# Performance work log

Measured on AMD Instinct MI355X. Metric: run time of the kernel, lower is better.

## Reference

```python
import jax, jax.numpy as jnp
import numpy as np

DIM = 256
HEADS = 8
HD = DIM // HEADS
SR = 2
SCALE = HD ** -0.5
EPS = 1e-5


def _layernorm(t, g, b):
    m = jnp.mean(t, axis=-1, keepdims=True)
    v = jnp.mean((t - m) ** 2, axis=-1, keepdims=True)
    return (t - m) / jnp.sqrt(v + EPS) * g + b


def _sr_kv(t, H, W, sr_w, sr_b, ln_g, ln_b, Wkv):
    # t: [B, N, C] with N == H*W -> spatial-reduction conv -> LN -> kv proj
    B, N, C = t.shape
    img = t.transpose(0, 2, 1).reshape(B, C, H, W)
    red = jax.lax.conv_general_dilated(
        img, sr_w, window_strides=(SR, SR), padding='VALID',
        dimension_numbers=('NCHW', 'OIHW', 'NCHW')) + sr_b[None, :, None, None]
    red = red.reshape(B, C, -1).transpose(0, 2, 1)  # [B, Nr, C]
    red = _layernorm(red, ln_g, ln_b)
    Nr = red.shape[1]
    kv = (red @ Wkv).reshape(B, Nr, 2, HEADS, HD).transpose(2, 0, 3, 1, 4)
    return kv[0], kv[1]  # k, v: [B, h, Nr, d]


def _q_heads(t, Wq):
    B, N, _ = t.shape
    return (t @ Wq).reshape(B, N, HEADS, HD).transpose(0, 2, 1, 3)  # [B,h,N,d]


def _attn_out(q, k, v, proj_w, proj_b):
    a = jnp.einsum('bhqd,bhkd->bhqk', q, k) * SCALE
    a = jax.nn.softmax(a, axis=-1)
    o = jnp.einsum('bhqk,bhkd->bhqd', a, v)
    B, h, N, d = o.shape
    return o.transpose(0, 2, 1, 3).reshape(B, N, h * d) @ proj_w + proj_b


def _forward(x, y, Wq, Wkv, sr_w, sr_b, ln_g, ln_b, proj_w, proj_b,
             H_x, W_x, H_y, W_y):
    # B_x == 1 branch of the original module (static shapes)
    B_y = y.shape[0]
    q_x = _q_heads(x, Wq)
    q_y = _q_heads(y, Wq)
    k_x, v_x = _sr_kv(x, H_x, W_x, sr_w, sr_b, ln_g, ln_b, Wkv)
    k_y, v_y = _sr_kv(y, H_y, W_y, sr_w, sr_b, ln_g, ln_b, Wkv)
    # x attends to its own KV + batch-averaged support KV
    k_cat_x = jnp.concatenate([k_x, jnp.mean(k_y, axis=0, keepdims=True)], axis=2)
    v_cat_x = jnp.concatenate([v_x, jnp.mean(v_y, axis=0, keepdims=True)], axis=2)
    x_out = _attn_out(q_x, k_cat_x, v_cat_x, proj_w, proj_b)
    # each support attends to repeated query KV + its own KV
    k_cat_y = jnp.concatenate([jnp.broadcast_to(k_x, (B_y,) + k_x.shape[1:]), k_y], axis=2)
    v_cat_y = jnp.concatenate([jnp.broadcast_to(v_x, (B_y,) + v_x.shape[1:]), v_y], axis=2)
    y_out = _attn_out(q_y, k_cat_y, v_cat_y, proj_w, proj_b)
    return x_out, y_out


def setup_inputs() -> dict:
    key = jax.random.key(0)
    ks = jax.random.split(key, 6)
    std = 0.02
    return {
        'x': jax.random.normal(ks[0], (1, 6400, DIM), jnp.float32),
        'y': jax.random.normal(ks[1], (4, 1024, DIM), jnp.float32),
        'Wq': jax.random.normal(ks[2], (DIM, DIM), jnp.float32) * std,
        'Wkv': jax.random.normal(ks[3], (DIM, 2 * DIM), jnp.float32) * std,
        'sr_w': jax.random.normal(ks[4], (DIM, DIM, SR, SR), jnp.float32) * np.sqrt(2.0 / (SR * SR * DIM)),
        'sr_b': jnp.zeros((DIM,), jnp.float32),
        'ln_g': jnp.ones((DIM,), jnp.float32),
        'ln_b': jnp.zeros((DIM,), jnp.float32),
        'proj_w': jax.random.normal(ks[5], (DIM, DIM), jnp.float32) * std,
        'proj_b': jnp.zeros((DIM,), jnp.float32),
        'H_x': 80, 'W_x': 80, 'H_y': 32, 'W_y': 32,
    }


def reference(x, y, Wq, Wkv, sr_w, sr_b, ln_g, ln_b, proj_w, proj_b,
              H_x, W_x, H_y, W_y):
    return _forward(x, y, Wq, Wkv, sr_w, sr_b, ln_g, ln_b, proj_w, proj_b,
                    H_x, W_x, H_y, W_y)
```

## Files before the change

### kernel.cpp

```cpp
#include <hip/hip_runtime.h>
#include <math.h>

#define DIM 256
#define HD 32
#define KSCALE (0.17677669529663687f * 1.44269504088896340736f)
#define EPS 1e-5f

typedef __attribute__((ext_vector_type(8))) short short8;
typedef __attribute__((ext_vector_type(4))) float f32x4;

union U8 { uint4 u; short8 s; };

__device__ inline unsigned short f2bf(float f) {
    union { float f; unsigned u; } v; v.f = f;
    unsigned r = v.u + 0x7FFF + ((v.u >> 16) & 1);
    return (unsigned short)(r >> 16);
}
__device__ inline float bf2f(unsigned short h) {
    union { unsigned u; float f; } v; v.u = ((unsigned)h) << 16;
    return v.f;
}
__device__ inline unsigned pk2bf(float a, float b) {
    unsigned ua = __float_as_uint(a) + 0x8000u;
    unsigned ub = __float_as_uint(b) + 0x8000u;
    return __builtin_amdgcn_perm(ub, ua, 0x07060302u);
}
__device__ inline uint4 pk8bf(float4 a, float4 b) {
    return make_uint4(pk2bf(a.x, a.y), pk2bf(a.z, a.w),
                      pk2bf(b.x, b.y), pk2bf(b.z, b.w));
}
__device__ inline void up2(unsigned u, float& a, float& b) {
    a = __uint_as_float(u << 16);
    b = __uint_as_float(u & 0xffff0000u);
}
__device__ inline void gl_lds16(const unsigned short* g, unsigned short* l) {
    __builtin_amdgcn_global_load_lds(
        (const __attribute__((address_space(1))) unsigned int*)g,
        (__attribute__((address_space(3))) unsigned int*)l, 16, 0, 0);
}
#define MFMA16(a, b, c) __builtin_amdgcn_mfma_f32_16x16x32_bf16(a, b, c, 0, 0, 0)
#define EXP2(x) __builtin_amdgcn_exp2f(x)

__global__ __launch_bounds__(256) void prep_w(
    const float* __restrict__ Wq, const float* __restrict__ Wkv,
    const float* __restrict__ projw, const float* __restrict__ srw,
    unsigned short* __restrict__ WqT, unsigned short* __restrict__ WkvT,
    unsigned short* __restrict__ projT, unsigned short* __restrict__ BwT)
{
    int idx = blockIdx.x * 256 + threadIdx.x;
    if (idx < 65536) { int n = idx >> 8, k = idx & 255; WqT[idx] = f2bf(Wq[(k << 8) + n]); return; }
    idx -= 65536;
    if (idx < 131072) { int n = idx >> 8, k = idx & 255; WkvT[idx] = f2bf(Wkv[(k << 9) + n]); return; }
    idx -= 131072;
    if (idx < 65536) { int n = idx >> 8, k = idx & 255; projT[idx] = f2bf(projw[(k << 8) + n]); return; }
    idx -= 65536;
    { int o = idx >> 10, rem = idx & 1023, q = rem >> 8, i = rem & 255;
      BwT[idx] = f2bf(srw[(o << 10) + (i << 2) + q]); }
}

__global__ __launch_bounds__(256) void convq_kernel(
    const float* __restrict__ x, const float* __restrict__ y,
    const unsigned short* __restrict__ BwT, const float* __restrict__ srb,
    const unsigned short* __restrict__ WqT,
    unsigned short* __restrict__ redx, unsigned short* __restrict__ redy,
    unsigned short* __restrict__ qxb, unsigned short* __restrict__ qyb)
{
    __shared__ __align__(16) unsigned short At[64][32];
    __shared__ __align__(16) unsigned short Btile[64][32];
    const int tid = threadIdx.x;
    const int lane = tid & 63, w = tid >> 6;
    const int c = lane & 15, quad = lane >> 4;
    const int srow = tid >> 2, sch = (tid & 3) << 3;
    const int bid = blockIdx.x;
    f32x4 acc[4] = {};
    const int rl = (w << 4) + (quad << 2);

    if (bid < 164) {
        const int n0 = (bid & 3) << 6, myi = bid >> 2;
        const float* Xb; unsigned short* Cb; int W, W2, m0;
        if (myi < 25) { Xb = x; Cb = redx; W = 80; W2 = 40; m0 = myi * 64; }
        else {
            const int r = myi - 25, b = r >> 2;
            Xb = y + (size_t)b * 262144; Cb = redy + (size_t)b * 65536;
            W = 32; W2 = 16; m0 = (r & 3) * 64;
        }
        const int p = m0 + srow;
        const int oy = p / W2, ox = p - oy * W2;
        const unsigned short* Bp = BwT + (size_t)(n0 + srow) * 1024 + sch;

        auto addrA = [&](int k0) {
            const int qq = k0 >> 8;
            const int rrow = (2 * oy + (qq >> 1)) * W + 2 * ox + (qq & 1);
            return Xb + (size_t)rrow * DIM + (k0 & 255) + sch;
        };

        const float* ap = addrA(0);
        float4 a0 = *(const float4*)ap, a1 = *(const float4*)(ap + 4);
        uint4 bn = *(const uint4*)Bp;
        for (int k0 = 0; k0 < 1024; k0 += 32) {
            *(uint4*)&At[srow][sch]    = pk8bf(a0, a1);
            *(uint4*)&Btile[srow][sch] = bn;
            if (k0 < 992) {
                const float* np = addrA(k0 + 32);
                a0 = *(const float4*)np; a1 = *(const float4*)(np + 4);
                bn = *(const uint4*)(Bp + k0 + 32);
            }
            __syncthreads();
            short8 a = *(short8*)&At[(w << 4) + c][quad << 3];
            #pragma unroll
            for (int nb = 0; nb < 4; ++nb) {
                short8 b = *(short8*)&Btile[(nb << 4) + c][quad << 3];
                acc[nb] = MFMA16(a, b, acc[nb]);
            }
            __syncthreads();
        }
        #pragma unroll
        for (int nb = 0; nb < 4; ++nb) {
            const int col = n0 + (nb << 4) + c;
            const float bv = srb[col];
            #pragma unroll
            for (int r = 0; r < 4; ++r)
                Cb[(size_t)(m0 + rl + r) * DIM + col] = f2bf(acc[nb][r] + bv);
        }
    } else {
        const int r = bid - 164;
        const int n0 = (r & 3) << 6, mg = (r >> 2) << 6;
        const float* Ab = (mg < 6400) ? x + (size_t)mg * 256
                                      : y + (size_t)(mg - 6400) * 256;
        unsigned short* Cb = (mg < 6400) ? qxb + (size_t)mg * 256
                                         : qyb + (size_t)(mg - 6400) * 256;
        const float* Ap = Ab + (size_t)srow * 256 + sch;
        const unsigned short* Bp = WqT + (size_t)(n0 + srow) * 256 + sch;

        float4 a0 = *(const float4*)Ap, a1 = *(const float4*)(Ap + 4);
        uint4 bn = *(const uint4*)Bp;
        for (int k0 = 0; k0 < 256; k0 += 32) {
            *(uint4*)&At[srow][sch]    = pk8bf(a0, a1);
            *(uint4*)&Btile[srow][sch] = bn;
            if (k0 < 224) {
                a0 = *(const float4*)(Ap + k0 + 32);
                a1 = *(const float4*)(Ap + k0 + 36);
                bn = *(const uint4*)(Bp + k0 + 32);
            }
            __syncthreads();
            short8 a = *(short8*)&At[(w << 4) + c][quad << 3];
            #pragma unroll
            for (int nb = 0; nb < 4; ++nb) {
                short8 b = *(short8*)&Btile[(nb << 4) + c][quad << 3];
                acc[nb] = MFMA16(a, b, acc[nb]);
            }
            __syncthreads();
        }
        #pragma unroll
        for (int nb = 0; nb < 4; ++nb) {
            const int col = n0 + (nb << 4) + c;
            #pragma unroll
            for (int r = 0; r < 4; ++r)
                Cb[(size_t)(rl + r) * 256 + col] = f2bf(acc[nb][r]);
        }
    }
}

__global__ __launch_bounds__(256) void kvln_kernel(
    const unsigned short* __restrict__ redx, const unsigned short* __restrict__ redy,
    const unsigned short* __restrict__ WkvT,
    const float* __restrict__ g, const float* __restrict__ bta,
    unsigned short* __restrict__ kswx, unsigned short* __restrict__ vswx,
    unsigned short* __restrict__ kswy, unsigned short* __restrict__ vswy)
{
    __shared__ __align__(16) unsigned short At[64][32];
    __shared__ __align__(16) unsigned short Btile[64][32];
    const int tid = threadIdx.x;
    const int lane = tid & 63, w = tid >> 6;
    const int c = lane & 15, quad = lane >> 4;
    const int srow = tid >> 2, sch = (tid & 3) << 3;
    const int bid = blockIdx.x;
    const int n0 = (bid & 7) << 6, mg = (bid >> 3) << 6;
    const unsigned short* Ab = (mg < 1600) ? redx + (size_t)mg * 256
                                           : redy + (size_t)(mg - 1600) * 256;
    const unsigned short* Arow = Ab + (size_t)srow * 256 + sch;

    uint4 araw[8];
    float s1 = 0.f, s2 = 0.f;
    #pragma unroll
    for (int ci = 0; ci < 8; ++ci) {
        araw[ci] = *(const uint4*)(Arow + (ci << 5));
        const unsigned* du = (const unsigned*)&araw[ci];
        #pragma unroll
        for (int dd = 0; dd < 4; ++dd) {
            float a, b; up2(du[dd], a, b);
            s1 += a + b; s2 += a * a + b * b;
        }
    }
    s1 += __shfl_xor(s1, 1); s1 += __shfl_xor(s1, 2);
    s2 += __shfl_xor(s2, 1); s2 += __shfl_xor(s2, 2);
    const float mean = s1 * (1.0f / 256.0f);
    const float var  = s2 * (1.0f / 256.0f) - mean * mean;
    const float rstd = rsqrtf(var + EPS);

    #pragma unroll
    for (int ci = 0; ci < 8; ++ci) {
        const int ch = (ci << 5) + sch;
        float4 g0 = *(const float4*)(g + ch),   g1 = *(const float4*)(g + ch + 4);
        float4 b0 = *(const float4*)(bta + ch), b1 = *(const float4*)(bta + ch + 4);
        const unsigned* du = (const unsigned*)&araw[ci];
        float v[8];
        #pragma unroll
        for (int dd = 0; dd < 4; ++dd) up2(du[dd], v[2 * dd], v[2 * dd + 1]);
        float4 o0 = make_float4(fmaf((v[0] - mean) * rstd, g0.x, b0.x),
                                fmaf((v[1] - mean) * rstd, g0.y, b0.y),
                                fmaf((v[2] - mean) * rstd, g0.z, b0.z),
                                fmaf((v[3] - mean) * rstd, g0.w, b0.w));
        float4 o1 = make_float4(fmaf((v[4] - mean) * rstd, g1.x, b1.x),
                                fmaf((v[5] - mean) * rstd, g1.y, b1.y),
                                fmaf((v[6] - mean) * rstd, g1.z, b1.z),
                                fmaf((v[7] - mean) * rstd, g1.w, b1.w));
        araw[ci] = pk8bf(o0, o1);
    }

    const unsigned short* Bp = WkvT + (size_t)(n0 + srow) * 256 + sch;
    uint4 bn = *(const uint4*)Bp;
    f32x4 acc[4] = {};
    for (int k0 = 0; k0 < 256; k0 += 32) {
        *(uint4*)&At[srow][sch]    = araw[k0 >> 5];
        *(uint4*)&Btile[srow][sch] = bn;
        if (k0 < 224) bn = *(const uint4*)(Bp + k0 + 32);
        __syncthreads();
        short8 a = *(short8*)&At[(w << 4) + c][quad << 3];
        #pragma unroll
        for (int nb = 0; nb < 4; ++nb) {
            short8 b = *(short8*)&Btile[(nb << 4) + c][quad << 3];
            acc[nb] = MFMA16(a, b, acc[nb]);
        }
        __syncthreads();
    }

    const int rl = (w << 4) + (quad << 2);
    const int r0 = mg - 1600;
    const int half = rl >> 5, kl0 = rl & 31;
    const int vkeyoff = (half << 10) + (((kl0 >> 2) & 3) << 7) + ((kl0 >> 4) << 2);
    #pragma unroll
    for (int nb = 0; nb < 4; ++nb) {
        const int col = n0 + (nb << 4) + c;
        if (col < 256) {
            const int hh = col >> 5, d = col & 31;
            unsigned short* base = (mg < 1600)
                ? kswx + ((size_t)(hh * 25 + (mg >> 6)) << 11)
                : kswy + ((size_t)(r0 >> 8) << 16) + ((size_t)((hh << 2) + ((r0 >> 6) & 3)) << 11);
            unsigned short* dst = base + (((d >> 3) << 9)) + (d & 7);
            #pragma unroll
            for (int r = 0; r < 4; ++r)
                dst[(rl + r) << 3] = f2bf(acc[nb][r] * KSCALE);
        } else {
            const int hd = col - 256, hv = hd >> 5, d = hd & 31;
            unsigned short* base = (mg < 1600)
                ? vswx + ((size_t)(hv * 25 + (mg >> 6)) << 11)
                : vswy + ((size_t)(r0 >> 8) << 16) + ((size_t)((hv << 2) + ((r0 >> 6) & 3)) << 11);
            unsigned lo = (unsigned)f2bf(acc[nb][0]) | ((unsigned)f2bf(acc[nb][1]) << 16);
            unsigned hi = (unsigned)f2bf(acc[nb][2]) | ((unsigned)f2bf(acc[nb][3]) << 16);
            *(uint2*)(base + vkeyoff + ((d >> 4) << 9) + ((d & 15) << 3)) =
                make_uint2(lo, hi);
        }
    }
}

__global__ __launch_bounds__(256) void kvmean_kernel(
    const unsigned short* __restrict__ kswy, const unsigned short* __restrict__ vswy,
    unsigned short* __restrict__ kmsw, unsigned short* __restrict__ vmsw)
{
    int idx = blockIdx.x * 256 + threadIdx.x;
    const unsigned short* s; unsigned short* dv; int e;
    if (idx < 65536) { s = kswy; dv = kmsw; e = idx; }
    else             { s = vswy; dv = vmsw; e = idx - 65536; }
    float sm = bf2f(s[e]) + bf2f(s[e + 65536]) + bf2f(s[e + 131072]) + bf2f(s[e + 196608]);
    dv[e] = f2bf(0.25f * sm);
}

__global__ __launch_bounds__(256) void attn_mfma(
    unsigned short* __restrict__ qxb, unsigned short* __restrict__ qyb,
    const unsigned short* __restrict__ kswx, const unsigned short* __restrict__ vswx,
    const unsigned short* __restrict__ kmsw, const unsigned short* __restrict__ vmsw,
    const unsigned short* __restrict__ kswy, const unsigned short* __restrict__ vswy,
    const unsigned short* __restrict__ kpad, const unsigned short* __restrict__ vpad)
{
    __shared__ __align__(16) unsigned short KV[2][8192];
    __shared__ __align__(16) float lsumLDS[4][64];

    const int tid = threadIdx.x;
    const int lane = tid & 63, w = tid >> 6;
    const int c = lane & 15, quad = lane >> 4;

    const int bid = blockIdx.x;
    unsigned short* qb; const unsigned short *k1, *v1, *k2, *v2;
    int h, qoff;
    if (bid < 800) {
        h = bid / 100; qoff = (bid - h * 100) * 64;
        qb = qxb;
        k1 = kswx + ((size_t)h * 25 << 11); v1 = vswx + ((size_t)h * 25 << 11);
        k2 = kmsw + ((size_t)h << 13);      v2 = vmsw + ((size_t)h << 13);
    } else {
        const int idx = bid - 800, b = idx >> 7, rem = idx & 127;
        h = rem >> 4; qoff = b * 1024 + (rem & 15) * 64;
        qb = qyb;
        k1 = kswx + ((size_t)h * 25 << 11); v1 = vswx + ((size_t)h * 25 << 11);
        k2 = kswy + ((size_t)b << 16) + ((size_t)h << 13);
        v2 = vswy + ((size_t)b << 16) + ((size_t)h << 13);
    }

    short8 qf[4];
    #pragma unroll
    for (int nb = 0; nb < 4; ++nb)
        qf[nb] = *(const short8*)(qb + (size_t)(qoff + (nb << 4) + c) * DIM
                                  + h * HD + (quad << 3));

    auto ksrc = [&](int t) -> const unsigned short* {
        if (t < 25) return k1 + (t << 11);
        if (t < 29) return k2 + ((t - 25) << 11);
        return kpad;
    };
    auto vsrc = [&](int t) -> const unsigned short* {
        if (t < 25) return v1 + (t << 11);
        if (t < 29) return v2 + ((t - 25) << 11);
        return vpad;
    };

    const int sg = (w << 9) + (lane << 3);
    auto stage = [&](int i, int pb) {
        #pragma unroll
        for (int tt = 0; tt < 2; ++tt) {
            const int t = 2 * i + tt;
            gl_lds16(ksrc(t) + sg, &KV[pb][(tt << 11) + (w << 9)]);
            gl_lds16(vsrc(t) + sg, &KV[pb][4096 + (tt << 11) + (w << 9)]);
        }
    };

    const int tb = w >> 1, half = w & 1;
    float lsr[4] = {0.f, 0.f, 0.f, 0.f};
    f32x4 oacc[4][2] = {};
    const f32x4 zero = {0.f, 0.f, 0.f, 0.f};

    stage(0, 0);
    __syncthreads();

    for (int i = 0; i < 15; ++i) {
        const int pb = i & 1;
        if (i < 14) stage(i + 1, pb ^ 1);

        const unsigned short* Kp = &KV[pb][(tb << 11) + (quad << 9) + (((half << 5) + c) << 3)];
        short8 ka0 = *(const short8*)(Kp);
        short8 ka1 = *(const short8*)(Kp + 128);
        f32x4 s0[4], s1[4];
        #pragma unroll
        for (int nb = 0; nb < 4; ++nb) s0[nb] = MFMA16(ka0, qf[nb], zero);
        #pragma unroll
        for (int nb = 0; nb < 4; ++nb) s1[nb] = MFMA16(ka1, qf[nb], zero);

        U8 af[4];
        #pragma unroll
        for (int nb = 0; nb < 4; ++nb) {
            float p0 = EXP2(s0[nb][0]), p1 = EXP2(s0[nb][1]);
            float p2 = EXP2(s0[nb][2]), p3 = EXP2(s0[nb][3]);
            float q0 = EXP2(s1[nb][0]), q1 = EXP2(s1[nb][1]);
            float q2 = EXP2(s1[nb][2]), q3 = EXP2(s1[nb][3]);
            lsr[nb] += ((p0 + p1) + (p2 + p3)) + ((q0 + q1) + (q2 + q3));
            af[nb].u = make_uint4(pk2bf(p0, p1), pk2bf(p2, p3),
                                  pk2bf(q0, q1), pk2bf(q2, q3));
        }

        const unsigned short* Vp = &KV[pb][4096 + (tb << 11) + (half << 10) + (quad << 7) + (c << 3)];
        short8 vb0 = *(const short8*)(Vp);
        short8 vb1 = *(const short8*)(Vp + 512);
        #pragma unroll
        for (int nb = 0; nb < 4; ++nb) {
            oacc[nb][0] = MFMA16(af[nb].s, vb0, oacc[nb][0]);
            oacc[nb][1] = MFMA16(af[nb].s, vb1, oacc[nb][1]);
        }

        __syncthreads();
    }

    #pragma unroll
    for (int nb = 0; nb < 4; ++nb) {
        lsr[nb] += __shfl_xor(lsr[nb], 16);
        lsr[nb] += __shfl_xor(lsr[nb], 32);
    }
    if (lane < 16) {
        #pragma unroll
        for (int nb = 0; nb < 4; ++nb) lsumLDS[w][(nb << 4) + lane] = lsr[nb];
    }
    float* Op = (float*)&KV[0][0];
    #pragma unroll
    for (int nb = 0; nb < 4; ++nb)
        #pragma unroll
        for (int db = 0; db < 2; ++db)
            *(f32x4*)&Op[((((w << 2) + nb) << 1) + db) * 256 + (c << 4) + (quad << 2)] =
                oacc[nb][db];
    __syncthreads();

    f32x4 lt = {0.f, 0.f, 0.f, 0.f};
    #pragma unroll
    for (int w2 = 0; w2 < 4; ++w2)
        lt += *(f32x4*)&lsumLDS[w2][(w << 4) + (quad << 2)];
    float inv[4];
    #pragma unroll
    for (int r = 0; r < 4; ++r) inv[r] = 1.0f / (lt[r] - 64.0f);
    #pragma unroll
    for (int db = 0; db < 2; ++db) {
        f32x4 o = zero;
        #pragma unroll
        for (int w2 = 0; w2 < 4; ++w2)
            o += *(f32x4*)&Op[((((w2 << 2) + w) << 1) + db) * 256 + (c << 4) + (quad << 2)];
        #pragma unroll
        for (int r = 0; r < 4; ++r) {
            const int row = qoff + (w << 4) + (quad << 2) + r;
            qb[(size_t)row * DIM + h * HD + (db << 4) + c] = f2bf(o[r] * inv[r]);
        }
    }
}

__global__ __launch_bounds__(256) void proj_mfma(
    const unsigned short* __restrict__ qxb, const unsigned short* __restrict__ qyb,
    const unsigned short* __restrict__ projT, const float* __restrict__ bias,
    float* __restrict__ outx, float* __restrict__ outy)
{
    __shared__ __align__(16) unsigned short At[64][32];
    __shared__ __align__(16) unsigned short Btile[64][32];
    const int tid = threadIdx.x;
    const int lane = tid & 63, w = tid >> 6;
    const int c = lane & 15, quad = lane >> 4;
    const int srow = tid >> 2, sch = (tid & 3) << 3;

    const int bid = blockIdx.x;
    const int n0 = (bid & 3) << 6, mg = (bid >> 2) << 6;
    const unsigned short* Ab = (mg < 6400) ? qxb + (size_t)mg * 256
                                           : qyb + (size_t)(mg - 6400) * 256;
    float* Cf = (mg < 6400) ? outx + (size_t)mg * 256 : outy + (size_t)(mg - 6400) * 256;

    const unsigned short* Ap = Ab + (size_t)srow * 256 + sch;
    const unsigned short* Bp = projT + (size_t)(n0 + srow) * 256 + sch;

    uint4 an = *(const uint4*)Ap, bn = *(const uint4*)Bp;
    f32x4 acc[4] = {};
    for (int k0 = 0; k0 < 256; k0 += 32) {
        *(uint4*)&At[srow][sch]    = an;
        *(uint4*)&Btile[srow][sch] = bn;
        if (k0 < 224) { an = *(const uint4*)(Ap + k0 + 32); bn = *(const uint4*)(Bp + k0 + 32); }
        __syncthreads();
        short8 a = *(short8*)&At[(w << 4) + c][quad << 3];
        #pragma unroll
        for (int nb = 0; nb < 4; ++nb) {
            short8 b = *(short8*)&Btile[(nb << 4) + c][quad << 3];
            acc[nb] = MFMA16(a, b, acc[nb]);
        }
        __syncthreads();
    }
    const int rl = (w << 4) + (quad << 2);
    #pragma unroll
    for (int nb = 0; nb < 4; ++nb) {
        const int col = n0 + (nb << 4) + c;
        const float bv = bias[col];
        #pragma unroll
        for (int r = 0; r < 4; ++r)
            Cf[(size_t)(rl + r) * 256 + col] = acc[nb][r] + bv;
    }
}

extern "C" void kernel_launch(void* const* d_in, const int* in_sizes, int n_in,
                              void* d_out, int out_size, void* d_ws, size_t ws_size,
                              hipStream_t stream)
{
    const float* x      = (const float*)d_in[0];
    const float* y      = (const float*)d_in[1];
    const float* Wq     = (const float*)d_in[2];
    const float* Wkv    = (const float*)d_in[3];
    const float* sr_w   = (const float*)d_in[4];
    const float* sr_b   = (const float*)d_in[5];
    const float* ln_g   = (const float*)d_in[6];
    const float* ln_b   = (const float*)d_in[7];
    const float* proj_w = (const float*)d_in[8];
    const float* proj_b = (const float*)d_in[9];

    unsigned short* p = (unsigned short*)d_ws;
    unsigned short* WqT   = p;  p += 65536;
    unsigned short* WkvT  = p;  p += 131072;
    unsigned short* projT = p;  p += 65536;
    unsigned short* BwT   = p;  p += 262144;
    unsigned short* redx  = p;  p += 409600;
    unsigned short* redy  = p;  p += 262144;
    unsigned short* qxb   = p;  p += 1638400;
    unsigned short* qyb   = p;  p += 1048576;
    unsigned short* kswx  = p;  p += 409600;
    unsigned short* vswx  = p;  p += 409600;
    unsigned short* kswy  = p;  p += 262144;
    unsigned short* vswy  = p;  p += 262144;
    unsigned short* kmsw  = p;  p += 65536;
    unsigned short* vmsw  = p;  p += 65536;
    unsigned short* kpad  = p;  p += 2048;
    unsigned short* vpad  = p;  p += 2048;
    float* outx = (float*)d_out;
    float* outy = outx + 6400 * 256;

    hipMemsetAsync(kpad, 0, 8192, stream);
    prep_w<<<2048, 256, 0, stream>>>(Wq, Wkv, proj_w, sr_w, WqT, WkvT, projT, BwT);
    convq_kernel<<<820, 256, 0, stream>>>(x, y, BwT, sr_b, WqT, redx, redy, qxb, qyb);
    kvln_kernel<<<328, 256, 0, stream>>>(redx, redy, WkvT, ln_g, ln_b,
                                         kswx, vswx, kswy, vswy);
    kvmean_kernel<<<512, 256, 0, stream>>>(kswy, vswy, kmsw, vmsw);
    attn_mfma<<<1312, 256, 0, stream>>>(qxb, qyb, kswx, vswx, kmsw, vmsw,
                                        kswy, vswy, kpad, vpad);
    proj_mfma<<<656, 256, 0, stream>>>(qxb, qyb, projT, proj_b, outx, outy);
}
```

Measured before the change: 169.8 us.

## Fuse Q projection into attention kernel and enlarge proj tile

Moves the Q = X·Wq projection out of the conv kernel and into the attention kernel, so each attention block computes its own 64x32 Q head slice with MFMA directly from fp32 inputs. This avoids writing and re-reading the bf16 Q buffer. The extra work is hidden behind the first KV stage load, and the conv kernel shrinks to the conv tiles only. The pad memset is folded into the weight-prep kernel, and the projection GEMM now uses 128-row tiles, halving its block count. The trade-off is that each attention block recomputes Q over K=256 reading fp32 x/y, giving 8x redundant reads of the x rows across heads.

```diff
diff --git a/kernel.cpp b/kernel.cpp
--- a/kernel.cpp
+++ b/kernel.cpp
@@ -45,7 +45,8 @@
     const float* __restrict__ Wq, const float* __restrict__ Wkv,
     const float* __restrict__ projw, const float* __restrict__ srw,
     unsigned short* __restrict__ WqT, unsigned short* __restrict__ WkvT,
-    unsigned short* __restrict__ projT, unsigned short* __restrict__ BwT)
+    unsigned short* __restrict__ projT, unsigned short* __restrict__ BwT,
+    unsigned short* __restrict__ pads)
 {
     int idx = blockIdx.x * 256 + threadIdx.x;
     if (idx < 65536) { int n = idx >> 8, k = idx & 255; WqT[idx] = f2bf(Wq[(k << 8) + n]); return; }
@@ -54,16 +55,16 @@
     idx -= 131072;
     if (idx < 65536) { int n = idx >> 8, k = idx & 255; projT[idx] = f2bf(projw[(k << 8) + n]); return; }
     idx -= 65536;
-    { int o = idx >> 10, rem = idx & 1023, q = rem >> 8, i = rem & 255;
-      BwT[idx] = f2bf(srw[(o << 10) + (i << 2) + q]); }
-}
-
-__global__ __launch_bounds__(256) void convq_kernel(
+    if (idx < 262144) { int o = idx >> 10, rem = idx & 1023, q = rem >> 8, i = rem & 255;
+                        BwT[idx] = f2bf(srw[(o << 10) + (i << 2) + q]); return; }
+    idx -= 262144;
+    pads[idx] = 0;
+}
+
+__global__ __launch_bounds__(256) void conv_kernel(
     const float* __restrict__ x, const float* __restrict__ y,
     const unsigned short* __restrict__ BwT, const float* __restrict__ srb,
-    const unsigned short* __restrict__ WqT,
-    unsigned short* __restrict__ redx, unsigned short* __restrict__ redy,
-    unsigned short* __restrict__ qxb, unsigned short* __restrict__ qyb)
+    unsigned short* __restrict__ redx, unsigned short* __restrict__ redy)
 {
     __shared__ __align__(16) unsigned short At[64][32];
     __shared__ __align__(16) unsigned short Btile[64][32];
@@ -75,89 +76,51 @@
     f32x4 acc[4] = {};
     const int rl = (w << 4) + (quad << 2);
 
-    if (bid < 164) {
-        const int n0 = (bid & 3) << 6, myi = bid >> 2;
-        const float* Xb; unsigned short* Cb; int W, W2, m0;
-        if (myi < 25) { Xb = x; Cb = redx; W = 80; W2 = 40; m0 = myi * 64; }
-        else {
-            const int r = myi - 25, b = r >> 2;
-            Xb = y + (size_t)b * 262144; Cb = redy + (size_t)b * 65536;
-            W = 32; W2 = 16; m0 = (r & 3) * 64;
-        }
-        const int p = m0 + srow;
-        const int oy = p / W2, ox = p - oy * W2;
-        const unsigned short* Bp = BwT + (size_t)(n0 + srow) * 1024 + sch;
-
-        auto addrA = [&](int k0) {
-            const int qq = k0 >> 8;
-            const int rrow = (2 * oy + (qq >> 1)) * W + 2 * ox + (qq & 1);
-            return Xb + (size_t)rrow * DIM + (k0 & 255) + sch;
-        };
-
-        const float* ap = addrA(0);
-        float4 a0 = *(const float4*)ap, a1 = *(const float4*)(ap + 4);
-        uint4 bn = *(const uint4*)Bp;
-        for (int k0 = 0; k0 < 1024; k0 += 32) {
-            *(uint4*)&At[srow][sch]    = pk8bf(a0, a1);
-            *(uint4*)&Btile[srow][sch] = bn;
-            if (k0 < 992) {
-                const float* np = addrA(k0 + 32);
-                a0 = *(const float4*)np; a1 = *(const float4*)(np + 4);
-                bn = *(const uint4*)(Bp + k0 + 32);
-            }
-            __syncthreads();
-            short8 a = *(short8*)&At[(w << 4) + c][quad << 3];
-            #pragma unroll
-            for (int nb = 0; nb < 4; ++nb) {
-                short8 b = *(short8*)&Btile[(nb << 4) + c][quad << 3];
-                acc[nb] = MFMA16(a, b, acc[nb]);
-            }
-            __syncthreads();
-        }
+    const int n0 = (bid & 3) << 6, myi = bid >> 2;
+    const float* Xb; unsigned short* Cb; int W, W2, m0;
+    if (myi < 25) { Xb = x; Cb = redx; W = 80; W2 = 40; m0 = myi * 64; }
+    else {
+        const int r = myi - 25, b = r >> 2;
+        Xb = y + (size_t)b * 262144; Cb = redy + (size_t)b * 65536;
+        W = 32; W2 = 16; m0 = (r & 3) * 64;
+    }
+    const int p = m0 + srow;
+    const int oy = p / W2, ox = p - oy * W2;
+    const unsigned short* Bp = BwT + (size_t)(n0 + srow) * 1024 + sch;
+
+    auto addrA = [&](int k0) {
+        const int qq = k0 >> 8;
+        const int rrow = (2 * oy + (qq >> 1)) * W + 2 * ox + (qq & 1);
+        return Xb + (size_t)rrow * DIM + (k0 & 255) + sch;
+    };
+
+    const float* ap = addrA(0);
+    float4 a0 = *(const float4*)ap, a1 = *(const float4*)(ap + 4);
+    uint4 bn = *(const uint4*)Bp;
+    for (int k0 = 0; k0 < 1024; k0 += 32) {
+        *(uint4*)&At[srow][sch]    = pk8bf(a0, a1);
+        *(uint4*)&Btile[srow][sch] = bn;
+        if (k0 < 992) {
+            const float* np = addrA(k0 + 32);
+            a0 = *(const float4*)np; a1 = *(const float4*)(np + 4);
+            bn = *(const uint4*)(Bp + k0 + 32);
+        }
+        __syncthreads();
+        short8 a = *(short8*)&At[(w << 4) + c][quad << 3];
         #pragma unroll
         for (int nb = 0; nb < 4; ++nb) {
-            const int col = n0 + (nb << 4) + c;
-            const float bv = srb[col];
-            #pragma unroll
-            for (int r = 0; r < 4; ++r)
-                Cb[(size_t)(m0 + rl + r) * DIM + col] = f2bf(acc[nb][r] + bv);
-        }
-    } else {
-        const int r = bid - 164;
-        const int n0 = (r & 3) << 6, mg = (r >> 2) << 6;
-        const float* Ab = (mg < 6400) ? x + (size_t)mg * 256
-                                      : y + (size_t)(mg - 6400) * 256;
-        unsigned short* Cb = (mg < 6400) ? qxb + (size_t)mg * 256
-                                         : qyb + (size_t)(mg - 6400) * 256;
-        const float* Ap = Ab + (size_t)srow * 256 + sch;
-        const unsigned short* Bp = WqT + (size_t)(n0 + srow) * 256 + sch;
-
-        float4 a0 = *(const float4*)Ap, a1 = *(const float4*)(Ap + 4);
-        uint4 bn = *(const uint4*)Bp;
-        for (int k0 = 0; k0 < 256; k0 += 32) {
-            *(uint4*)&At[srow][sch]    = pk8bf(a0, a1);
-            *(uint4*)&Btile[srow][sch] = bn;
-            if (k0 < 224) {
-                a0 = *(const float4*)(Ap + k0 + 32);
-                a1 = *(const float4*)(Ap + k0 + 36);
-                bn = *(const uint4*)(Bp + k0 + 32);
-            }
-            __syncthreads();
-            short8 a = *(short8*)&At[(w << 4) + c][quad << 3];
-            #pragma unroll
-            for (int nb = 0; nb < 4; ++nb) {
-                short8 b = *(short8*)&Btile[(nb << 4) + c][quad << 3];
-                acc[nb] = MFMA16(a, b, acc[nb]);
-            }
-            __syncthreads();
-        }
-        #pragma unroll
-        for (int nb = 0; nb < 4; ++nb) {
-            const int col = n0 + (nb << 4) + c;
-            #pragma unroll
-            for (int r = 0; r < 4; ++r)
-                Cb[(size_t)(rl + r) * 256 + col] = f2bf(acc[nb][r]);
-        }
+            short8 b = *(short8*)&Btile[(nb << 4) + c][quad << 3];
+            acc[nb] = MFMA16(a, b, acc[nb]);
+        }
+        __syncthreads();
+    }
+    #pragma unroll
+    for (int nb = 0; nb < 4; ++nb) {
+        const int col = n0 + (nb << 4) + c;
+        const float bv = srb[col];
+        #pragma unroll
+        for (int r = 0; r < 4; ++r)
+            Cb[(size_t)(m0 + rl + r) * DIM + col] = f2bf(acc[nb][r] + bv);
     }
 }
 
@@ -277,13 +240,16 @@
 }
 
 __global__ __launch_bounds__(256) void attn_mfma(
-    unsigned short* __restrict__ qxb, unsigned short* __restrict__ qyb,
+    const float* __restrict__ xf, const float* __restrict__ yf,
+    const unsigned short* __restrict__ WqT,
+    unsigned short* __restrict__ obx, unsigned short* __restrict__ oby,
     const unsigned short* __restrict__ kswx, const unsigned short* __restrict__ vswx,
     const unsigned short* __restrict__ kmsw, const unsigned short* __restrict__ vmsw,
     const unsigned short* __restrict__ kswy, const unsigned short* __restrict__ vswy,
     const unsigned short* __restrict__ kpad, const unsigned short* __restrict__ vpad)
 {
     __shared__ __align__(16) unsigned short KV[2][8192];
+    __shared__ __align__(16) unsigned short Qbuf[64][40];
     __shared__ __align__(16) float lsumLDS[4][64];
 
     const int tid = threadIdx.x;
@@ -291,27 +257,22 @@
     const int c = lane & 15, quad = lane >> 4;
 
     const int bid = blockIdx.x;
-    unsigned short* qb; const unsigned short *k1, *v1, *k2, *v2;
+    const float* qsrc; unsigned short* ob;
+    const unsigned short *k1, *v1, *k2, *v2;
     int h, qoff;
     if (bid < 800) {
         h = bid / 100; qoff = (bid - h * 100) * 64;
-        qb = qxb;
+        qsrc = xf; ob = obx;
         k1 = kswx + ((size_t)h * 25 << 11); v1 = vswx + ((size_t)h * 25 << 11);
         k2 = kmsw + ((size_t)h << 13);      v2 = vmsw + ((size_t)h << 13);
     } else {
         const int idx = bid - 800, b = idx >> 7, rem = idx & 127;
         h = rem >> 4; qoff = b * 1024 + (rem & 15) * 64;
-        qb = qyb;
+        qsrc = yf; ob = oby;
         k1 = kswx + ((size_t)h * 25 << 11); v1 = vswx + ((size_t)h * 25 << 11);
         k2 = kswy + ((size_t)b << 16) + ((size_t)h << 13);
         v2 = vswy + ((size_t)b << 16) + ((size_t)h << 13);
     }
-
-    short8 qf[4];
-    #pragma unroll
-    for (int nb = 0; nb < 4; ++nb)
-        qf[nb] = *(const short8*)(qb + (size_t)(qoff + (nb << 4) + c) * DIM
-                                  + h * HD + (quad << 3));
 
     auto ksrc = [&](int t) -> const unsigned short* {
         if (t < 25) return k1 + (t << 11);
@@ -323,7 +284,6 @@
         if (t < 29) return v2 + ((t - 25) << 11);
         return vpad;
     };
-
     const int sg = (w << 9) + (lane << 3);
     auto stage = [&](int i, int pb) {
         #pragma unroll
@@ -334,13 +294,40 @@
         }
     };
 
+    const f32x4 zero = {0.f, 0.f, 0.f, 0.f};
+
+    stage(0, 0);
+
+    {
+        const float* xr = qsrc + (size_t)(qoff + (w << 4) + c) * DIM;
+        const unsigned short* wqA = WqT + (size_t)(h * HD + c) * DIM + (quad << 3);
+        f32x4 qa0 = zero, qa1 = zero;
+        #pragma unroll
+        for (int kk = 0; kk < 8; ++kk) {
+            const int ko = (kk << 5) + (quad << 3);
+            float4 b0 = *(const float4*)(xr + ko);
+            float4 b1 = *(const float4*)(xr + ko + 4);
+            U8 bfr; bfr.u = pk8bf(b0, b1);
+            short8 a0 = *(const short8*)(wqA + (kk << 5));
+            short8 a1 = *(const short8*)(wqA + 16 * DIM + (kk << 5));
+            qa0 = MFMA16(a0, bfr.s, qa0);
+            qa1 = MFMA16(a1, bfr.s, qa1);
+        }
+        *(uint2*)&Qbuf[(w << 4) + c][(quad << 2)] =
+            make_uint2(pk2bf(qa0[0], qa0[1]), pk2bf(qa0[2], qa0[3]));
+        *(uint2*)&Qbuf[(w << 4) + c][16 + (quad << 2)] =
+            make_uint2(pk2bf(qa1[0], qa1[1]), pk2bf(qa1[2], qa1[3]));
+    }
+    __syncthreads();
+
+    short8 qf[4];
+    #pragma unroll
+    for (int nb = 0; nb < 4; ++nb)
+        qf[nb] = *(const short8*)&Qbuf[(nb << 4) + c][quad << 3];
+
     const int tb = w >> 1, half = w & 1;
     float lsr[4] = {0.f, 0.f, 0.f, 0.f};
     f32x4 oacc[4][2] = {};
-    const f32x4 zero = {0.f, 0.f, 0.f, 0.f};
-
-    stage(0, 0);
-    __syncthreads();
 
     for (int i = 0; i < 15; ++i) {
         const int pb = i & 1;
@@ -413,55 +400,68 @@
         #pragma unroll
         for (int r = 0; r < 4; ++r) {
             const int row = qoff + (w << 4) + (quad << 2) + r;
-            qb[(size_t)row * DIM + h * HD + (db << 4) + c] = f2bf(o[r] * inv[r]);
+            ob[(size_t)row * DIM + h * HD + (db << 4) + c] = f2bf(o[r] * inv[r]);
         }
     }
 }
 
 __global__ __launch_bounds__(256) void proj_mfma(
-    const unsigned short* __restrict__ qxb, const unsigned short* __restrict__ qyb,
+    const unsigned short* __restrict__ obx, const unsigned short* __restrict__ oby,
     const unsigned short* __restrict__ projT, const float* __restrict__ bias,
     float* __restrict__ outx, float* __restrict__ outy)
 {
-    __shared__ __align__(16) unsigned short At[64][32];
+    __shared__ __align__(16) unsigned short At[128][32];
     __shared__ __align__(16) unsigned short Btile[64][32];
     const int tid = threadIdx.x;
     const int lane = tid & 63, w = tid >> 6;
     const int c = lane & 15, quad = lane >> 4;
-    const int srow = tid >> 2, sch = (tid & 3) << 3;
 
     const int bid = blockIdx.x;
-    const int n0 = (bid & 3) << 6, mg = (bid >> 2) << 6;
-    const unsigned short* Ab = (mg < 6400) ? qxb + (size_t)mg * 256
-                                           : qyb + (size_t)(mg - 6400) * 256;
+    const int n0 = (bid & 3) << 6, mg = (bid >> 2) << 7;
+    const unsigned short* Ab = (mg < 6400) ? obx + (size_t)mg * 256
+                                           : oby + (size_t)(mg - 6400) * 256;
     float* Cf = (mg < 6400) ? outx + (size_t)mg * 256 : outy + (size_t)(mg - 6400) * 256;
 
-    const unsigned short* Ap = Ab + (size_t)srow * 256 + sch;
-    const unsigned short* Bp = projT + (size_t)(n0 + srow) * 256 + sch;
-
-    uint4 an = *(const uint4*)Ap, bn = *(const uint4*)Bp;
-    f32x4 acc[4] = {};
+    const int arow = tid >> 1, ach = (tid & 1) << 4;
+    const unsigned short* Ap = Ab + (size_t)arow * 256 + ach;
+    const int brow = tid >> 2, bch = (tid & 3) << 3;
+    const unsigned short* Bp = projT + (size_t)(n0 + brow) * 256 + bch;
+
+    uint4 an0 = *(const uint4*)Ap, an1 = *(const uint4*)(Ap + 8);
+    uint4 bn  = *(const uint4*)Bp;
+    f32x4 acc[2][4] = {};
     for (int k0 = 0; k0 < 256; k0 += 32) {
-        *(uint4*)&At[srow][sch]    = an;
-        *(uint4*)&Btile[srow][sch] = bn;
-        if (k0 < 224) { an = *(const uint4*)(Ap + k0 + 32); bn = *(const uint4*)(Bp + k0 + 32); }
-        __syncthreads();
-        short8 a = *(short8*)&At[(w << 4) + c][quad << 3];
+        *(uint4*)&At[arow][ach]     = an0;
+        *(uint4*)&At[arow][ach + 8] = an1;
+        *(uint4*)&Btile[brow][bch]  = bn;
+        if (k0 < 224) {
+            an0 = *(const uint4*)(Ap + k0 + 32);
+            an1 = *(const uint4*)(Ap + k0 + 40);
+            bn  = *(const uint4*)(Bp + k0 + 32);
+        }
+        __syncthreads();
+        #pragma unroll
+        for (int ml = 0; ml < 2; ++ml) {
+            short8 a = *(short8*)&At[(w << 5) + (ml << 4) + c][quad << 3];
+            #pragma unroll
+            for (int nb = 0; nb < 4; ++nb) {
+                short8 b = *(short8*)&Btile[(nb << 4) + c][quad << 3];
+                acc[ml][nb] = MFMA16(a, b, acc[ml][nb]);
+            }
+        }
+        __syncthreads();
+    }
+    #pragma unroll
+    for (int ml = 0; ml < 2; ++ml) {
+        const int rl = (w << 5) + (ml << 4) + (quad << 2);
         #pragma unroll
         for (int nb = 0; nb < 4; ++nb) {
-            short8 b = *(short8*)&Btile[(nb << 4) + c][quad << 3];
-            acc[nb] = MFMA16(a, b, acc[nb]);
-        }
-        __syncthreads();
-    }
-    const int rl = (w << 4) + (quad << 2);
-    #pragma unroll
-    for (int nb = 0; nb < 4; ++nb) {
-        const int col = n0 + (nb << 4) + c;
-        const float bv = bias[col];
-        #pragma unroll
-        for (int r = 0; r < 4; ++r)
-            Cf[(size_t)(rl + r) * 256 + col] = acc[nb][r] + bv;
+            const int col = n0 + (nb << 4) + c;
+            const float bv = bias[col];
+            #pragma unroll
+            for (int r = 0; r < 4; ++r)
+                Cf[(size_t)(rl + r) * 256 + col] = acc[ml][nb][r] + bv;
+        }
     }
 }
 
@@ -487,8 +487,8 @@
     unsigned short* BwT   = p;  p += 262144;
     unsigned short* redx  = p;  p += 409600;
     unsigned short* redy  = p;  p += 262144;
-    unsigned short* qxb   = p;  p += 1638400;
-    unsigned short* qyb   = p;  p += 1048576;
+    unsigned short* obx   = p;  p += 1638400;
+    unsigned short* oby   = p;  p += 1048576;
     unsigned short* kswx  = p;  p += 409600;
     unsigned short* vswx  = p;  p += 409600;
     unsigned short* kswy  = p;  p += 262144;
@@ -500,13 +500,12 @@
     float* outx = (float*)d_out;
     float* outy = outx + 6400 * 256;
 
-    hipMemsetAsync(kpad, 0, 8192, stream);
-    prep_w<<<2048, 256, 0, stream>>>(Wq, Wkv, proj_w, sr_w, WqT, WkvT, projT, BwT);
-    convq_kernel<<<820, 256, 0, stream>>>(x, y, BwT, sr_b, WqT, redx, redy, qxb, qyb);
+    prep_w<<<2064, 256, 0, stream>>>(Wq, Wkv, proj_w, sr_w, WqT, WkvT, projT, BwT, kpad);
+    conv_kernel<<<164, 256, 0, stream>>>(x, y, BwT, sr_b, redx, redy);
     kvln_kernel<<<328, 256, 0, stream>>>(redx, redy, WkvT, ln_g, ln_b,
                                          kswx, vswx, kswy, vswy);
     kvmean_kernel<<<512, 256, 0, stream>>>(kswy, vswy, kmsw, vmsw);
-    attn_mfma<<<1312, 256, 0, stream>>>(qxb, qyb, kswx, vswx, kmsw, vmsw,
-                                        kswy, vswy, kpad, vpad);
-    proj_mfma<<<656, 256, 0, stream>>>(qxb, qyb, projT, proj_b, outx, outy);
-}
+    attn_mfma<<<1312, 256, 0, stream>>>(x, y, WqT, obx, oby, kswx, vswx,
+                                        kmsw, vmsw, kswy, vswy, kpad, vpad);
+    proj_mfma<<<328, 256, 0, stream>>>(obx, oby, projT, proj_b, outx, outy);
+}
```

Result: slower. 179.1 us (+5.4%).

## Split-K the SR conv, fold pad zeroing into prep, enlarge q/proj GEMM tiles

Applied to the files above, without the earlier changes.

The spatial-reduction conv GEMM is split into two K halves written to separate buffers, doubling its block count. kvln then sums the halves and adds the conv bias before LayerNorm. The q-projection and output-projection GEMMs now use 128-row tiles with two M subtiles per wave, halving block counts and reusing B tiles more. The pad memset moves into prep_w to drop a launch; partial sums are rounded to bf16 separately, adding slight precision loss and extra traffic.

```diff
diff --git a/kernel.cpp b/kernel.cpp
--- a/kernel.cpp
+++ b/kernel.cpp
@@ -45,7 +45,8 @@
     const float* __restrict__ Wq, const float* __restrict__ Wkv,
     const float* __restrict__ projw, const float* __restrict__ srw,
     unsigned short* __restrict__ WqT, unsigned short* __restrict__ WkvT,
-    unsigned short* __restrict__ projT, unsigned short* __restrict__ BwT)
+    unsigned short* __restrict__ projT, unsigned short* __restrict__ BwT,
+    unsigned short* __restrict__ pads)
 {
     int idx = blockIdx.x * 256 + threadIdx.x;
     if (idx < 65536) { int n = idx >> 8, k = idx & 255; WqT[idx] = f2bf(Wq[(k << 8) + n]); return; }
@@ -54,39 +55,43 @@
     idx -= 131072;
     if (idx < 65536) { int n = idx >> 8, k = idx & 255; projT[idx] = f2bf(projw[(k << 8) + n]); return; }
     idx -= 65536;
-    { int o = idx >> 10, rem = idx & 1023, q = rem >> 8, i = rem & 255;
-      BwT[idx] = f2bf(srw[(o << 10) + (i << 2) + q]); }
+    if (idx < 262144) { int o = idx >> 10, rem = idx & 1023, q = rem >> 8, i = rem & 255;
+                        BwT[idx] = f2bf(srw[(o << 10) + (i << 2) + q]); return; }
+    idx -= 262144;
+    pads[idx] = 0;
 }
 
 __global__ __launch_bounds__(256) void convq_kernel(
     const float* __restrict__ x, const float* __restrict__ y,
-    const unsigned short* __restrict__ BwT, const float* __restrict__ srb,
-    const unsigned short* __restrict__ WqT,
-    unsigned short* __restrict__ redx, unsigned short* __restrict__ redy,
+    const unsigned short* __restrict__ BwT, const unsigned short* __restrict__ WqT,
+    unsigned short* __restrict__ redA, unsigned short* __restrict__ redB,
     unsigned short* __restrict__ qxb, unsigned short* __restrict__ qyb)
 {
-    __shared__ __align__(16) unsigned short At[64][32];
+    __shared__ __align__(16) unsigned short At[128][32];
     __shared__ __align__(16) unsigned short Btile[64][32];
     const int tid = threadIdx.x;
     const int lane = tid & 63, w = tid >> 6;
     const int c = lane & 15, quad = lane >> 4;
-    const int srow = tid >> 2, sch = (tid & 3) << 3;
     const int bid = blockIdx.x;
-    f32x4 acc[4] = {};
-    const int rl = (w << 4) + (quad << 2);
-
-    if (bid < 164) {
-        const int n0 = (bid & 3) << 6, myi = bid >> 2;
-        const float* Xb; unsigned short* Cb; int W, W2, m0;
-        if (myi < 25) { Xb = x; Cb = redx; W = 80; W2 = 40; m0 = myi * 64; }
-        else {
-            const int r = myi - 25, b = r >> 2;
-            Xb = y + (size_t)b * 262144; Cb = redy + (size_t)b * 65536;
-            W = 32; W2 = 16; m0 = (r & 3) * 64;
-        }
-        const int p = m0 + srow;
+
+    if (bid < 328) {
+        const int n0 = (bid & 3) << 6, r = bid >> 2;
+        const float* Xb; int W, W2, m0g, pl, kh;
+        if (r < 50) {
+            const int myi = r >> 1; kh = r & 1;
+            Xb = x; W = 80; W2 = 40; m0g = myi * 64; pl = myi * 64;
+        } else {
+            const int ry = r - 50, idx = ry >> 1; kh = ry & 1;
+            const int b = idx >> 2, mt = idx & 3;
+            Xb = y + (size_t)b * 262144; W = 32; W2 = 16;
+            m0g = 1600 + b * 256 + mt * 64; pl = mt * 64;
+        }
+        unsigned short* Cb = (kh == 0) ? redA : redB;
+        const int srow = tid >> 2, sch = (tid & 3) << 3;
+        const int p = pl + srow;
         const int oy = p / W2, ox = p - oy * W2;
         const unsigned short* Bp = BwT + (size_t)(n0 + srow) * 1024 + sch;
+        const int kbeg = kh << 9, kend = kbeg + 512;
 
         auto addrA = [&](int k0) {
             const int qq = k0 >> 8;
@@ -94,13 +99,14 @@
             return Xb + (size_t)rrow * DIM + (k0 & 255) + sch;
         };
 
-        const float* ap = addrA(0);
+        const float* ap = addrA(kbeg);
         float4 a0 = *(const float4*)ap, a1 = *(const float4*)(ap + 4);
-        uint4 bn = *(const uint4*)Bp;
-        for (int k0 = 0; k0 < 1024; k0 += 32) {
+        uint4 bn = *(const uint4*)(Bp + kbeg);
+        f32x4 acc[4] = {};
+        for (int k0 = kbeg; k0 < kend; k0 += 32) {
             *(uint4*)&At[srow][sch]    = pk8bf(a0, a1);
             *(uint4*)&Btile[srow][sch] = bn;
-            if (k0 < 992) {
+            if (k0 < kend - 32) {
                 const float* np = addrA(k0 + 32);
                 a0 = *(const float4*)np; a1 = *(const float4*)(np + 4);
                 bn = *(const uint4*)(Bp + k0 + 32);
@@ -114,56 +120,68 @@
             }
             __syncthreads();
         }
+        const int rl = (w << 4) + (quad << 2);
         #pragma unroll
         for (int nb = 0; nb < 4; ++nb) {
             const int col = n0 + (nb << 4) + c;
-            const float bv = srb[col];
-            #pragma unroll
-            for (int r = 0; r < 4; ++r)
-                Cb[(size_t)(m0 + rl + r) * DIM + col] = f2bf(acc[nb][r] + bv);
+            #pragma unroll
+            for (int rr = 0; rr < 4; ++rr)
+                Cb[(size_t)(m0g + rl + rr) * DIM + col] = f2bf(acc[nb][rr]);
         }
     } else {
-        const int r = bid - 164;
-        const int n0 = (r & 3) << 6, mg = (r >> 2) << 6;
+        const int r = bid - 328;
+        const int n0 = (r & 3) << 6, mg = (r >> 2) << 7;
         const float* Ab = (mg < 6400) ? x + (size_t)mg * 256
                                       : y + (size_t)(mg - 6400) * 256;
         unsigned short* Cb = (mg < 6400) ? qxb + (size_t)mg * 256
                                          : qyb + (size_t)(mg - 6400) * 256;
-        const float* Ap = Ab + (size_t)srow * 256 + sch;
-        const unsigned short* Bp = WqT + (size_t)(n0 + srow) * 256 + sch;
-
-        float4 a0 = *(const float4*)Ap, a1 = *(const float4*)(Ap + 4);
+        const int arow = tid >> 1, ach = (tid & 1) << 4;
+        const float* Ap = Ab + (size_t)arow * 256 + ach;
+        const int brow = tid >> 2, bch = (tid & 3) << 3;
+        const unsigned short* Bp = WqT + (size_t)(n0 + brow) * 256 + bch;
+
+        float4 a0 = *(const float4*)Ap,       a1 = *(const float4*)(Ap + 4);
+        float4 a2 = *(const float4*)(Ap + 8), a3 = *(const float4*)(Ap + 12);
         uint4 bn = *(const uint4*)Bp;
+        f32x4 acc[2][4] = {};
         for (int k0 = 0; k0 < 256; k0 += 32) {
-            *(uint4*)&At[srow][sch]    = pk8bf(a0, a1);
-            *(uint4*)&Btile[srow][sch] = bn;
+            *(uint4*)&At[arow][ach]     = pk8bf(a0, a1);
+            *(uint4*)&At[arow][ach + 8] = pk8bf(a2, a3);
+            *(uint4*)&Btile[brow][bch]  = bn;
             if (k0 < 224) {
-                a0 = *(const float4*)(Ap + k0 + 32);
-                a1 = *(const float4*)(Ap + k0 + 36);
+                a0 = *(const float4*)(Ap + k0 + 32); a1 = *(const float4*)(Ap + k0 + 36);
+                a2 = *(const float4*)(Ap + k0 + 40); a3 = *(const float4*)(Ap + k0 + 44);
                 bn = *(const uint4*)(Bp + k0 + 32);
             }
             __syncthreads();
-            short8 a = *(short8*)&At[(w << 4) + c][quad << 3];
-            #pragma unroll
-            for (int nb = 0; nb < 4; ++nb) {
-                short8 b = *(short8*)&Btile[(nb << 4) + c][quad << 3];
-                acc[nb] = MFMA16(a, b, acc[nb]);
+            #pragma unroll
+            for (int ml = 0; ml < 2; ++ml) {
+                short8 a = *(short8*)&At[(w << 5) + (ml << 4) + c][quad << 3];
+                #pragma unroll
+                for (int nb = 0; nb < 4; ++nb) {
+                    short8 b = *(short8*)&Btile[(nb << 4) + c][quad << 3];
+                    acc[ml][nb] = MFMA16(a, b, acc[ml][nb]);
+                }
             }
             __syncthreads();
         }
         #pragma unroll
-        for (int nb = 0; nb < 4; ++nb) {
-            const int col = n0 + (nb << 4) + c;
-            #pragma unroll
-            for (int r = 0; r < 4; ++r)
-                Cb[(size_t)(rl + r) * 256 + col] = f2bf(acc[nb][r]);
+        for (int ml = 0; ml < 2; ++ml) {
+            const int rl = (w << 5) + (ml << 4) + (quad << 2);
+            #pragma unroll
+            for (int nb = 0; nb < 4; ++nb) {
+                const int col = n0 + (nb << 4) + c;
+                #pragma unroll
+                for (int rr = 0; rr < 4; ++rr)
+                    Cb[(size_t)(rl + rr) * 256 + col] = f2bf(acc[ml][nb][rr]);
+            }
         }
     }
 }
 
 __global__ __launch_bounds__(256) void kvln_kernel(
-    const unsigned short* __restrict__ redx, const unsigned short* __restrict__ redy,
-    const unsigned short* __restrict__ WkvT,
+    const unsigned short* __restrict__ redA, const unsigned short* __restrict__ redB,
+    const unsigned short* __restrict__ WkvT, const float* __restrict__ srb,
     const float* __restrict__ g, const float* __restrict__ bta,
     unsigned short* __restrict__ kswx, unsigned short* __restrict__ vswx,
     unsigned short* __restrict__ kswy, unsigned short* __restrict__ vswy)
@@ -176,21 +194,33 @@
     const int srow = tid >> 2, sch = (tid & 3) << 3;
     const int bid = blockIdx.x;
     const int n0 = (bid & 7) << 6, mg = (bid >> 3) << 6;
-    const unsigned short* Ab = (mg < 1600) ? redx + (size_t)mg * 256
-                                           : redy + (size_t)(mg - 1600) * 256;
-    const unsigned short* Arow = Ab + (size_t)srow * 256 + sch;
+    const unsigned short* ArowA = redA + (size_t)(mg + srow) * 256 + sch;
+    const unsigned short* ArowB = redB + (size_t)(mg + srow) * 256 + sch;
 
     uint4 araw[8];
     float s1 = 0.f, s2 = 0.f;
     #pragma unroll
     for (int ci = 0; ci < 8; ++ci) {
-        araw[ci] = *(const uint4*)(Arow + (ci << 5));
-        const unsigned* du = (const unsigned*)&araw[ci];
+        uint4 ua = *(const uint4*)(ArowA + (ci << 5));
+        uint4 ub = *(const uint4*)(ArowB + (ci << 5));
+        const int ch = (ci << 5) + sch;
+        float4 sb0 = *(const float4*)(srb + ch), sb1 = *(const float4*)(srb + ch + 4);
+        const unsigned* dua = (const unsigned*)&ua;
+        const unsigned* dub = (const unsigned*)&ub;
+        float t[8];
         #pragma unroll
         for (int dd = 0; dd < 4; ++dd) {
-            float a, b; up2(du[dd], a, b);
-            s1 += a + b; s2 += a * a + b * b;
-        }
+            float a0, a1, b0, b1;
+            up2(dua[dd], a0, a1); up2(dub[dd], b0, b1);
+            t[2 * dd]     = a0 + b0;
+            t[2 * dd + 1] = a1 + b1;
+        }
+        t[0] += sb0.x; t[1] += sb0.y; t[2] += sb0.z; t[3] += sb0.w;
+        t[4] += sb1.x; t[5] += sb1.y; t[6] += sb1.z; t[7] += sb1.w;
+        #pragma unroll
+        for (int j = 0; j < 8; ++j) { s1 += t[j]; s2 += t[j] * t[j]; }
+        araw[ci] = pk8bf(make_float4(t[0], t[1], t[2], t[3]),
+                         make_float4(t[4], t[5], t[6], t[7]));
     }
     s1 += __shfl_xor(s1, 1); s1 += __shfl_xor(s1, 2);
     s2 += __shfl_xor(s2, 1); s2 += __shfl_xor(s2, 2);
@@ -423,45 +453,58 @@
     const unsigned short* __restrict__ projT, const float* __restrict__ bias,
     float* __restrict__ outx, float* __restrict__ outy)
 {
-    __shared__ __align__(16) unsigned short At[64][32];
+    __shared__ __align__(16) unsigned short At[128][32];
     __shared__ __align__(16) unsigned short Btile[64][32];
     const int tid = threadIdx.x;
     const int lane = tid & 63, w = tid >> 6;
     const int c = lane & 15, quad = lane >> 4;
-    const int srow = tid >> 2, sch = (tid & 3) << 3;
 
     const int bid = blockIdx.x;
-    const int n0 = (bid & 3) << 6, mg = (bid >> 2) << 6;
+    const int n0 = (bid & 3) << 6, mg = (bid >> 2) << 7;
     const unsigned short* Ab = (mg < 6400) ? qxb + (size_t)mg * 256
                                            : qyb + (size_t)(mg - 6400) * 256;
     float* Cf = (mg < 6400) ? outx + (size_t)mg * 256 : outy + (size_t)(mg - 6400) * 256;
 
-    const unsigned short* Ap = Ab + (size_t)srow * 256 + sch;
-    const unsigned short* Bp = projT + (size_t)(n0 + srow) * 256 + sch;
-
-    uint4 an = *(const uint4*)Ap, bn = *(const uint4*)Bp;
-    f32x4 acc[4] = {};
+    const int arow = tid >> 1, ach = (tid & 1) << 4;
+    const unsigned short* Ap = Ab + (size_t)arow * 256 + ach;
+    const int brow = tid >> 2, bch = (tid & 3) << 3;
+    const unsigned short* Bp = projT + (size_t)(n0 + brow) * 256 + bch;
+
+    uint4 an0 = *(const uint4*)Ap, an1 = *(const uint4*)(Ap + 8);
+    uint4 bn  = *(const uint4*)Bp;
+    f32x4 acc[2][4] = {};
     for (int k0 = 0; k0 < 256; k0 += 32) {
-        *(uint4*)&At[srow][sch]    = an;
-        *(uint4*)&Btile[srow][sch] = bn;
-        if (k0 < 224) { an = *(const uint4*)(Ap + k0 + 32); bn = *(const uint4*)(Bp + k0 + 32); }
+        *(uint4*)&At[arow][ach]     = an0;
+        *(uint4*)&At[arow][ach + 8] = an1;
+        *(uint4*)&Btile[brow][bch]  = bn;
+        if (k0 < 224) {
+            an0 = *(const uint4*)(Ap + k0 + 32);
+            an1 = *(const uint4*)(Ap + k0 + 40);
+            bn  = *(const uint4*)(Bp + k0 + 32);
+        }
         __syncthreads();
-        short8 a = *(short8*)&At[(w << 4) + c][quad << 3];
+        #pragma unroll
+        for (int ml = 0; ml < 2; ++ml) {
+            short8 a = *(short8*)&At[(w << 5) + (ml << 4) + c][quad << 3];
+            #pragma unroll
+            for (int nb = 0; nb < 4; ++nb) {
+                short8 b = *(short8*)&Btile[(nb << 4) + c][quad << 3];
+                acc[ml][nb] = MFMA16(a, b, acc[ml][nb]);
+            }
+        }
+        __syncthreads();
+    }
+    #pragma unroll
+    for (int ml = 0; ml < 2; ++ml) {
+        const int rl = (w << 5) + (ml << 4) + (quad << 2);
         #pragma unroll
         for (int nb = 0; nb < 4; ++nb) {
-            short8 b = *(short8*)&Btile[(nb << 4) + c][quad << 3];
-            acc[nb] = MFMA16(a, b, acc[nb]);
-        }
-        __syncthreads();
-    }
-    const int rl = (w << 4) + (quad << 2);
-    #pragma unroll
-    for (int nb = 0; nb < 4; ++nb) {
-        const int col = n0 + (nb << 4) + c;
-        const float bv = bias[col];
-        #pragma unroll
-        for (int r = 0; r < 4; ++r)
-            Cf[(size_t)(rl + r) * 256 + col] = acc[nb][r] + bv;
+            const int col = n0 + (nb << 4) + c;
+            const float bv = bias[col];
+            #pragma unroll
+            for (int r = 0; r < 4; ++r)
+                Cf[(size_t)(rl + r) * 256 + col] = acc[ml][nb][r] + bv;
+        }
     }
 }
 
@@ -485,8 +528,8 @@
     unsigned short* WkvT  = p;  p += 131072;
     unsigned short* projT = p;  p += 65536;
     unsigned short* BwT   = p;  p += 262144;
-    unsigned short* redx  = p;  p += 409600;
-    unsigned short* redy  = p;  p += 262144;
+    unsigned short* redA  = p;  p += 671744;
+    unsigned short* redB  = p;  p += 671744;
     unsigned short* qxb   = p;  p += 1638400;
     unsigned short* qyb   = p;  p += 1048576;
     unsigned short* kswx  = p;  p += 409600;
@@ -500,13 +543,12 @@
     float* outx = (float*)d_out;
     float* outy = outx + 6400 * 256;
 
-    hipMemsetAsync(kpad, 0, 8192, stream);
-    prep_w<<<2048, 256, 0, stream>>>(Wq, Wkv, proj_w, sr_w, WqT, WkvT, projT, BwT);
-    convq_kernel<<<820, 256, 0, stream>>>(x, y, BwT, sr_b, WqT, redx, redy, qxb, qyb);
-    kvln_kernel<<<328, 256, 0, stream>>>(redx, redy, WkvT, ln_g, ln_b,
+    prep_w<<<2064, 256, 0, stream>>>(Wq, Wkv, proj_w, sr_w, WqT, WkvT, projT, BwT, kpad);
+    convq_kernel<<<656, 256, 0, stream>>>(x, y, BwT, WqT, redA, redB, qxb, qyb);
+    kvln_kernel<<<328, 256, 0, stream>>>(redA, redB, WkvT, sr_b, ln_g, ln_b,
                                          kswx, vswx, kswy, vswy);
     kvmean_kernel<<<512, 256, 0, stream>>>(kswy, vswy, kmsw, vmsw);
     attn_mfma<<<1312, 256, 0, stream>>>(qxb, qyb, kswx, vswx, kmsw, vmsw,
                                         kswy, vswy, kpad, vpad);
-    proj_mfma<<<656, 256, 0, stream>>>(qxb, qyb, projT, proj_b, outx, outy);
-}
+    proj_mfma<<<328, 256, 0, stream>>>(qxb, qyb, projT, proj_b, outx, outy);
+}
```

Result: no change. 166.6 us (-1.9%).
